# Optimization experiments

Hardware: AMD Instinct MI355X
Metric: run time of the kernel (lower is better)

The kernel has to match this reference:

```python
import jax, jax.numpy as jnp
import numpy as np

# ---- Hash-grid configuration (matches init_kwargs / torch-ngp HashEncoder) ----
L = 16            # num_levels
D = 2             # level_dim
BASE = 16         # base_resolution
DESIRED = 2048    # desired_resolution
MAXP = 2 ** 19    # 2**log2_hashmap_size
DIVIDE = 1.5

S = np.exp2(np.log2(DESIRED / BASE) / (L - 1))          # per-level scale ~1.3819
RES = np.ceil(BASE * S ** np.arange(L)).astype(np.int64)  # [L] grid resolutions
_sizes = np.minimum(MAXP, (RES + 1) ** 3)
SIZES = (np.ceil(_sizes / 8) * 8).astype(np.int64)       # aligned to 8, per torch-ngp
OFFSETS = np.concatenate([[0], np.cumsum(SIZES)[:-1]])
TOTAL = int(SIZES.sum())  # 6119864
DENSE = (RES + 1) ** 3 <= SIZES                          # levels small enough for direct index
PRIMES = (1, 2654435761, 805459861)


def hash_encode(x01, table):
    """x01: [N,3] in [0,1]; table: [TOTAL, D]. Returns [N, L*D]."""
    N = x01.shape[0]
    scale = jnp.asarray(BASE * S ** np.arange(L) - 1.0, jnp.float32)   # [L]
    pos = x01[:, None, :] * scale[None, :, None] + 0.5                 # [N,L,3]
    pg_f = jnp.floor(pos)
    frac = pos - pg_f                                                  # [N,L,3]
    pg = pg_f.astype(jnp.uint32)

    res1 = jnp.asarray(RES + 1, jnp.uint32)        # [L]
    sizes = jnp.asarray(SIZES, jnp.uint32)         # [L]
    offs = jnp.asarray(OFFSETS, jnp.int32)         # [L]
    dense = jnp.asarray(DENSE)                     # [L] bool

    feat = jnp.zeros((N, L, D), x01.dtype)
    for c in range(8):  # 8 trilinear corners (fixed small loop)
        bit = np.array([(c >> 0) & 1, (c >> 1) & 1, (c >> 2) & 1])
        cg = pg + jnp.asarray(bit, jnp.uint32)                         # [N,L,3]
        w = jnp.prod(jnp.where(jnp.asarray(bit.astype(bool)), frac, 1.0 - frac), axis=-1)  # [N,L]
        idx_dense = cg[..., 0] + cg[..., 1] * res1 + cg[..., 2] * res1 * res1
        h = (cg[..., 0] * jnp.uint32(PRIMES[0])) ^ (cg[..., 1] * jnp.uint32(PRIMES[1])) ^ (cg[..., 2] * jnp.uint32(PRIMES[2]))
        idx = jnp.where(dense[None, :], idx_dense % sizes, h % sizes)  # [N,L]
        gidx = idx.astype(jnp.int32) + offs[None, :]                   # global table index
        feat = feat + w[..., None] * table[gidx]                       # gather + lerp accumulate
    return feat.reshape(N, L * D)


def setup_inputs() -> dict:
    key = jax.random.key(0)
    ks = jax.random.split(key, 10)
    N = 524288
    x = jax.random.uniform(ks[0], (N, 3), jnp.float32)                # coords in [0,1)
    table = jax.random.uniform(ks[1], (TOTAL, D), jnp.float32, -1e-4, 1e-4)
    def lin(k, fi, fo):
        return jax.random.normal(k, (fi, fo), jnp.float32) / np.sqrt(fi)
    return {
        'x': x, 'table': table,
        'w1': lin(ks[2], 32, 256), 'b1': jnp.zeros((256,), jnp.float32),
        'w2': lin(ks[3], 256, 256), 'b2': jnp.zeros((256,), jnp.float32),
        'w3': lin(ks[4], 256, 256), 'b3': jnp.zeros((256,), jnp.float32),
        'w4': lin(ks[5], 256, 3), 'b4': jnp.zeros((3,), jnp.float32),
    }


def reference(x, table, w1, b1, w2, b2, w3, b3, w4, b4):
    feat = hash_encode(x / DIVIDE, table)                 # [N,32]
    h = jax.nn.relu(feat @ w1 + b1)
    h = jax.nn.relu(h @ w2 + b2)
    h = jax.nn.relu(h @ w3 + b3)
    rgb = jax.nn.sigmoid(h @ w4 + b4)                     # [N,3]
    return rgb
```

## Files before the change

### kernel.cpp

```cpp
#include <hip/hip_runtime.h>
#include <hip/hip_bf16.h>
#include <math.h>

#define NTHREADS 256
#define BR 64

typedef __attribute__((ext_vector_type(8))) short   s16x8;
typedef __attribute__((ext_vector_type(8))) __bf16  bf16x8;
typedef __attribute__((ext_vector_type(4))) float   f32x4;

__device__ __constant__ float c_scale[16] = {
    15.0f,        21.110607f,  29.554930f,  41.224254f,
    57.350239f,   79.634946f,  110.430473f, 152.987205f,
    211.796890f,  293.066769f, 405.374657f, 560.574388f,
    775.046906f,  1071.429232f, 1481.003616f, 2047.0f
};
__device__ __constant__ unsigned c_off[16] = {
    0u,        4920u,     18744u,    51512u,
    136696u,   352696u,   876984u,   1401272u,
    1925560u,  2449848u,  2974136u,  3498424u,
    4022712u,  4547000u,  5071288u,  5595576u
};
__device__ __constant__ unsigned c_res1[16] = {
    17u, 24u, 32u, 44u, 60u, 0u,0u,0u,0u,0u,0u,0u,0u,0u,0u,0u
};

__device__ inline unsigned short f2bf(float f) {
    unsigned u = __builtin_bit_cast(unsigned, f);
    u += 0x7FFFu + ((u >> 16) & 1u);
    return (unsigned short)(u >> 16);
}
__device__ inline float bf2f(unsigned short h) {
    unsigned u = ((unsigned)h) << 16;
    return __builtin_bit_cast(float, u);
}
__device__ inline f32x4 mfma_bf16(s16x8 a, s16x8 b, f32x4 c) {
    return __builtin_amdgcn_mfma_f32_16x16x32_bf16(
        __builtin_bit_cast(bf16x8, a), __builtin_bit_cast(bf16x8, b), c, 0, 0, 0);
}

__global__ void convert_w(const float* __restrict__ w1, const float* __restrict__ w2,
                          const float* __restrict__ w3, unsigned short* __restrict__ ws) {
    int t = blockIdx.x * blockDim.x + threadIdx.x;
    if (t < 8192) {
        int col = t >> 5, k = t & 31;
        ws[t] = f2bf(w1[k * 256 + col]);
    } else if (t < 73728) {
        int u = t - 8192; int col = u >> 8, k = u & 255;
        ws[t] = f2bf(w2[k * 256 + col]);
    } else if (t < 139264) {
        int u = t - 73728; int col = u >> 8, k = u & 255;
        ws[t] = f2bf(w3[k * 256 + col]);
    }
}

__global__ void convert_table(const float* __restrict__ t, unsigned short* __restrict__ o, int n4) {
    int i = blockIdx.x * blockDim.x + threadIdx.x;
    if (i < n4) {
        float4 v = ((const float4*)t)[i];
        ushort4 r;
        r.x = f2bf(v.x); r.y = f2bf(v.y); r.z = f2bf(v.z); r.w = f2bf(v.w);
        ((ushort4*)o)[i] = r;
    }
}

__global__ __launch_bounds__(256)
void encode_kernel(const float* __restrict__ x, const unsigned short* __restrict__ tbf,
                   uint2* __restrict__ feat2, int N)
{
    const int p  = blockIdx.x * 256 + threadIdx.x;
    const int lp = blockIdx.y;
    if (p >= N) return;

    const float inv = (1.0f / 1.5f);
    const float xc = x[3 * p + 0] * inv;
    const float yc = x[3 * p + 1] * inv;
    const float zc = x[3 * p + 2] * inv;

    unsigned outv[2];
    #pragma unroll
    for (int s = 0; s < 2; ++s) {
        const int l = lp * 2 + s;
        const float sc = c_scale[l];
        const float px = xc * sc + 0.5f;
        const float py = yc * sc + 0.5f;
        const float pz = zc * sc + 0.5f;
        const float fx = floorf(px), fy = floorf(py), fz = floorf(pz);
        const float rx = px - fx, ry = py - fy, rz = pz - fz;
        const unsigned ux = (unsigned)fx, uy = (unsigned)fy, uz = (unsigned)fz;
        const unsigned off = c_off[l];
        const unsigned r1  = c_res1[l];
        const bool dense = (l < 5);
        float ax = 0.0f, ay = 0.0f;
        #pragma unroll
        for (int c = 0; c < 8; ++c) {
            const unsigned bx = c & 1, by = (c >> 1) & 1, bz = (c >> 2) & 1;
            const unsigned cx = ux + bx, cy = uy + by, cz = uz + bz;
            const float wx = bx ? rx : (1.0f - rx);
            const float wy = by ? ry : (1.0f - ry);
            const float wz = bz ? rz : (1.0f - rz);
            const float w = wx * wy * wz;
            unsigned idx;
            if (dense) idx = cx + cy * r1 + cz * r1 * r1;
            else       idx = (cx ^ (cy * 2654435761u) ^ (cz * 805459861u)) & 524287u;
            const unsigned v = *reinterpret_cast<const unsigned*>(tbf + 2u * (idx + off));
            ax = fmaf(w, bf2f((unsigned short)(v & 0xFFFFu)), ax);
            ay = fmaf(w, bf2f((unsigned short)(v >> 16)), ay);
        }
        outv[s] = (unsigned)f2bf(ax) | ((unsigned)f2bf(ay) << 16);
    }
    feat2[(size_t)lp * N + p] = make_uint2(outv[0], outv[1]);
}

__global__ __launch_bounds__(NTHREADS, 3)
void mlp_kernel(const uint2* __restrict__ feat2,
                const unsigned short* __restrict__ wt,
                const float* __restrict__ b1, const float* __restrict__ b2,
                const float* __restrict__ b3,
                const float* __restrict__ w4, const float* __restrict__ b4,
                float* __restrict__ out, int N)
{
    __shared__ unsigned short sA[BR * 256];
    char* sAb = (char*)sA;

    const int tid = threadIdx.x;
    const int p0  = blockIdx.x * BR;
    if (p0 >= N) return;

    #pragma unroll
    for (int it = 0; it < 2; ++it) {
        const int t  = it * NTHREADS + tid;
        const int lp = t >> 6;
        const int p  = t & 63;
        const uint2 v = feat2[(size_t)lp * N + p0 + p];
        *reinterpret_cast<uint2*>(
            sAb + p * 512 + (((unsigned)(lp * 8)) ^ ((unsigned)((p & 7) << 4)))) = v;
    }
    __syncthreads();

    const int lane = tid & 63;
    const int wid  = tid >> 6;
    const int rowb = wid * 64;
    const int arow = lane & 15;
    const int kgrp = lane >> 4;
    const int bcol = lane & 15;

    f32x4 acc[4][4];

    auto epilogue = [&](const float* __restrict__ bias) {
        #pragma unroll
        for (int rt = 0; rt < 4; ++rt) {
            const int f0 = rowb + rt * 16 + kgrp * 4;
            const float4 bv = *reinterpret_cast<const float4*>(bias + f0);
            #pragma unroll
            for (int ct = 0; ct < 4; ++ct) {
                const int p = ct * 16 + bcol;
                const float v0 = fmaxf(acc[rt][ct][0] + bv.x, 0.0f);
                const float v1 = fmaxf(acc[rt][ct][1] + bv.y, 0.0f);
                const float v2 = fmaxf(acc[rt][ct][2] + bv.z, 0.0f);
                const float v3 = fmaxf(acc[rt][ct][3] + bv.w, 0.0f);
                uint2 pk;
                pk.x = (unsigned)f2bf(v0) | ((unsigned)f2bf(v1) << 16);
                pk.y = (unsigned)f2bf(v2) | ((unsigned)f2bf(v3) << 16);
                *reinterpret_cast<uint2*>(
                    sAb + p * 512 + (((unsigned)(2 * f0)) ^ ((unsigned)((p & 7) << 4)))) = pk;
            }
        }
    };

    {
        #pragma unroll
        for (int rt = 0; rt < 4; ++rt)
            #pragma unroll
            for (int ct = 0; ct < 4; ++ct) acc[rt][ct] = f32x4{0.f, 0.f, 0.f, 0.f};

        s16x8 wfr[4];
        #pragma unroll
        for (int rt = 0; rt < 4; ++rt)
            wfr[rt] = *reinterpret_cast<const s16x8*>(wt + (rowb + rt * 16 + arow) * 32 + kgrp * 8);
        #pragma unroll
        for (int ct = 0; ct < 4; ++ct) {
            const int p = ct * 16 + bcol;
            const s16x8 bfr = *reinterpret_cast<const s16x8*>(
                sAb + p * 512 + (((unsigned)(kgrp * 16)) ^ ((unsigned)((p & 7) << 4))));
            #pragma unroll
            for (int rt = 0; rt < 4; ++rt)
                acc[rt][ct] = mfma_bf16(wfr[rt], bfr, acc[rt][ct]);
        }
        __syncthreads();
        epilogue(b1);
        __syncthreads();
    }

    #pragma unroll 1
    for (int layer = 0; layer < 2; ++layer) {
        const unsigned short* __restrict__ W = wt + 8192 + (layer << 16);
        #pragma unroll
        for (int rt = 0; rt < 4; ++rt)
            #pragma unroll
            for (int ct = 0; ct < 4; ++ct) acc[rt][ct] = f32x4{0.f, 0.f, 0.f, 0.f};

        for (int ks = 0; ks < 8; ++ks) {
            s16x8 wfr[4];
            #pragma unroll
            for (int rt = 0; rt < 4; ++rt)
                wfr[rt] = *reinterpret_cast<const s16x8*>(
                    W + (rowb + rt * 16 + arow) * 256 + ks * 32 + kgrp * 8);
            #pragma unroll
            for (int ct = 0; ct < 4; ++ct) {
                const int p = ct * 16 + bcol;
                const s16x8 bfr = *reinterpret_cast<const s16x8*>(
                    sAb + p * 512 + (((unsigned)(ks * 64 + kgrp * 16)) ^ ((unsigned)((p & 7) << 4))));
                #pragma unroll
                for (int rt = 0; rt < 4; ++rt)
                    acc[rt][ct] = mfma_bf16(wfr[rt], bfr, acc[rt][ct]);
            }
        }
        __syncthreads();
        epilogue(layer == 0 ? b2 : b3);
        __syncthreads();
    }

    if (tid < BR * 3) {
        const int r = tid / 3;
        const int c = tid - 3 * r;
        float z = 0.0f;
        for (int kb = 0; kb < 32; ++kb) {
            const s16x8 hv = *reinterpret_cast<const s16x8*>(
                sAb + r * 512 + (((unsigned)(kb * 16)) ^ ((unsigned)((r & 7) << 4))));
            #pragma unroll
            for (int j = 0; j < 8; ++j)
                z = fmaf(bf2f((unsigned short)hv[j]), w4[(kb * 8 + j) * 3 + c], z);
        }
        z += b4[c];
        const int pi = p0 + r;
        if (pi < N) out[pi * 3 + c] = 1.0f / (1.0f + expf(-z));
    }
}

template<bool BFT>
__global__ __launch_bounds__(NTHREADS, 3)
void fused_hashmlp(const float* __restrict__ x, const float* __restrict__ table,
                   const unsigned short* __restrict__ tbf,
                   const unsigned short* __restrict__ wt,
                   const float* __restrict__ b1, const float* __restrict__ b2,
                   const float* __restrict__ b3,
                   const float* __restrict__ w4, const float* __restrict__ b4,
                   float* __restrict__ out, int N)
{
    __shared__ float sX[BR][3];
    __shared__ unsigned short sA[BR * 256];
    const int tid = threadIdx.x;
    const int p0  = blockIdx.x * BR;
    if (p0 >= N) return;
    char* sAb = (char*)sA;

    if (tid < BR * 3) sX[tid / 3][tid % 3] = x[p0 * 3 + tid];
    __syncthreads();

    #pragma unroll
    for (int it = 0; it < 4; ++it) {
        const int task = it * NTHREADS + tid;
        const int l = task >> 6;
        const int p = task & 63;
        const float sc  = c_scale[l];
        const float inv = (1.0f / 1.5f);
        const float px = sX[p][0] * inv * sc + 0.5f;
        const float py = sX[p][1] * inv * sc + 0.5f;
        const float pz = sX[p][2] * inv * sc + 0.5f;
        const float fx = floorf(px), fy = floorf(py), fz = floorf(pz);
        const float rx = px - fx, ry = py - fy, rz = pz - fz;
        const unsigned ux = (unsigned)fx, uy = (unsigned)fy, uz = (unsigned)fz;
        const unsigned off = c_off[l];
        const unsigned r1  = c_res1[l];
        const bool dense = (l < 5);
        float ax = 0.0f, ay = 0.0f;
        #pragma unroll
        for (int c = 0; c < 8; ++c) {
            const unsigned bx = c & 1, by = (c >> 1) & 1, bz = (c >> 2) & 1;
            const unsigned cx = ux + bx, cy = uy + by, cz = uz + bz;
            const float wx = bx ? rx : (1.0f - rx);
            const float wy = by ? ry : (1.0f - ry);
            const float wz = bz ? rz : (1.0f - rz);
            const float w = wx * wy * wz;
            unsigned idx;
            if (dense) idx = cx + cy * r1 + cz * r1 * r1;
            else       idx = (cx ^ (cy * 2654435761u) ^ (cz * 805459861u)) & 524287u;
            float tx, ty;
            if (BFT) {
                const unsigned v = *reinterpret_cast<const unsigned*>(tbf + 2u * (idx + off));
                tx = bf2f((unsigned short)(v & 0xFFFFu));
                ty = bf2f((unsigned short)(v >> 16));
            } else {
                const float2 tv = *reinterpret_cast<const float2*>(table + 2u * (idx + off));
                tx = tv.x; ty = tv.y;
            }
            ax = fmaf(w, tx, ax);
            ay = fmaf(w, ty, ay);
        }
        const unsigned pack = (unsigned)f2bf(ax) | ((unsigned)f2bf(ay) << 16);
        *reinterpret_cast<unsigned*>(sAb + p * 512 + ((l * 4) ^ ((p & 7) << 4))) = pack;
    }
    __syncthreads();

    const int lane = tid & 63;
    const int wid  = tid >> 6;
    const int rowb = wid * 64;
    const int arow = lane & 15;
    const int kgrp = lane >> 4;
    const int bcol = lane & 15;

    f32x4 acc[4][4];

    auto epilogue = [&](const float* __restrict__ bias) {
        #pragma unroll
        for (int rt = 0; rt < 4; ++rt) {
            const int f0 = rowb + rt * 16 + kgrp * 4;
            const float4 bv = *reinterpret_cast<const float4*>(bias + f0);
            #pragma unroll
            for (int ct = 0; ct < 4; ++ct) {
                const int p = ct * 16 + bcol;
                const float v0 = fmaxf(acc[rt][ct][0] + bv.x, 0.0f);
                const float v1 = fmaxf(acc[rt][ct][1] + bv.y, 0.0f);
                const float v2 = fmaxf(acc[rt][ct][2] + bv.z, 0.0f);
                const float v3 = fmaxf(acc[rt][ct][3] + bv.w, 0.0f);
                uint2 pk;
                pk.x = (unsigned)f2bf(v0) | ((unsigned)f2bf(v1) << 16);
                pk.y = (unsigned)f2bf(v2) | ((unsigned)f2bf(v3) << 16);
                *reinterpret_cast<uint2*>(
                    sAb + p * 512 + (((unsigned)(2 * f0)) ^ ((unsigned)((p & 7) << 4)))) = pk;
            }
        }
    };

    {
        #pragma unroll
        for (int rt = 0; rt < 4; ++rt)
            #pragma unroll
            for (int ct = 0; ct < 4; ++ct) acc[rt][ct] = f32x4{0.f, 0.f, 0.f, 0.f};
        s16x8 wfr[4];
        #pragma unroll
        for (int rt = 0; rt < 4; ++rt)
            wfr[rt] = *reinterpret_cast<const s16x8*>(wt + (rowb + rt * 16 + arow) * 32 + kgrp * 8);
        #pragma unroll
        for (int ct = 0; ct < 4; ++ct) {
            const int p = ct * 16 + bcol;
            const s16x8 bfr = *reinterpret_cast<const s16x8*>(
                sAb + p * 512 + (((unsigned)(kgrp * 16)) ^ ((unsigned)((p & 7) << 4))));
            #pragma unroll
            for (int rt = 0; rt < 4; ++rt)
                acc[rt][ct] = mfma_bf16(wfr[rt], bfr, acc[rt][ct]);
        }
        __syncthreads();
        epilogue(b1);
        __syncthreads();
    }

    #pragma unroll 1
    for (int layer = 0; layer < 2; ++layer) {
        const unsigned short* __restrict__ W = wt + 8192 + (layer << 16);
        #pragma unroll
        for (int rt = 0; rt < 4; ++rt)
            #pragma unroll
            for (int ct = 0; ct < 4; ++ct) acc[rt][ct] = f32x4{0.f, 0.f, 0.f, 0.f};
        for (int ks = 0; ks < 8; ++ks) {
            s16x8 wfr[4];
            #pragma unroll
            for (int rt = 0; rt < 4; ++rt)
                wfr[rt] = *reinterpret_cast<const s16x8*>(
                    W + (rowb + rt * 16 + arow) * 256 + ks * 32 + kgrp * 8);
            #pragma unroll
            for (int ct = 0; ct < 4; ++ct) {
                const int p = ct * 16 + bcol;
                const s16x8 bfr = *reinterpret_cast<const s16x8*>(
                    sAb + p * 512 + (((unsigned)(ks * 64 + kgrp * 16)) ^ ((unsigned)((p & 7) << 4))));
                #pragma unroll
                for (int rt = 0; rt < 4; ++rt)
                    acc[rt][ct] = mfma_bf16(wfr[rt], bfr, acc[rt][ct]);
            }
        }
        __syncthreads();
        epilogue(layer == 0 ? b2 : b3);
        __syncthreads();
    }

    if (tid < BR * 3) {
        const int r = tid / 3;
        const int c = tid - 3 * r;
        float z = 0.0f;
        for (int kb = 0; kb < 32; ++kb) {
            const s16x8 hv = *reinterpret_cast<const s16x8*>(
                sAb + r * 512 + (((unsigned)(kb * 16)) ^ ((unsigned)((r & 7) << 4))));
            #pragma unroll
            for (int j = 0; j < 8; ++j)
                z = fmaf(bf2f((unsigned short)hv[j]), w4[(kb * 8 + j) * 3 + c], z);
        }
        z += b4[c];
        const int pi = p0 + r;
        if (pi < N) out[pi * 3 + c] = 1.0f / (1.0f + expf(-z));
    }
}

extern "C" void kernel_launch(void* const* d_in, const int* in_sizes, int n_in,
                              void* d_out, int out_size, void* d_ws, size_t ws_size,
                              hipStream_t stream) {
    const float* x     = (const float*)d_in[0];
    const float* table = (const float*)d_in[1];
    const float* w1    = (const float*)d_in[2];
    const float* b1    = (const float*)d_in[3];
    const float* w2    = (const float*)d_in[4];
    const float* b2    = (const float*)d_in[5];
    const float* w3    = (const float*)d_in[6];
    const float* b3    = (const float*)d_in[7];
    const float* w4    = (const float*)d_in[8];
    const float* b4    = (const float*)d_in[9];
    float* out = (float*)d_out;

    const int N = in_sizes[0] / 3;

    const size_t W_ELEMS    = 139264;
    const size_t TBL_ELEMS  = 12239728;
    const size_t need_bf    = (W_ELEMS + TBL_ELEMS) * 2;
    const size_t FEAT_BYTES = (size_t)N * 64;
    const size_t need_split = need_bf + FEAT_BYTES;

    unsigned short* wsw = (unsigned short*)d_ws;
    unsigned short* tbf = wsw + W_ELEMS;
    uint2* feat2 = (uint2*)((char*)d_ws + need_bf);

    hipLaunchKernelGGL(convert_w, dim3(544), dim3(256), 0, stream, w1, w2, w3, wsw);

    if (ws_size >= need_split) {
        const size_t n4 = TBL_ELEMS / 4;
        hipLaunchKernelGGL(convert_table, dim3((unsigned)((n4 + 255) / 256)), dim3(256), 0, stream,
                           table, tbf, (int)n4);
        hipLaunchKernelGGL(encode_kernel, dim3((N + 255) / 256, 8), dim3(256), 0, stream,
                           x, tbf, feat2, N);
        hipLaunchKernelGGL(mlp_kernel, dim3((N + BR - 1) / BR), dim3(NTHREADS), 0, stream,
                           feat2, wsw, b1, b2, b3, w4, b4, out, N);
    } else if (ws_size >= need_bf) {
        const size_t n4 = TBL_ELEMS / 4;
        hipLaunchKernelGGL(convert_table, dim3((unsigned)((n4 + 255) / 256)), dim3(256), 0, stream,
                           table, tbf, (int)n4);
        hipLaunchKernelGGL(fused_hashmlp<true>, dim3((N + BR - 1) / BR), dim3(NTHREADS), 0, stream,
                           x, table, tbf, wsw, b1, b2, b3, w4, b4, out, N);
    } else {
        hipLaunchKernelGGL(fused_hashmlp<false>, dim3((N + BR - 1) / BR), dim3(NTHREADS), 0, stream,
                           x, table, tbf, wsw, b1, b2, b3, w4, b4, out, N);
    }
}
```

Measured before the change: 664.8 us.

## Use MFMA for output layer, packed bf16 converts, interleave encode block order

The final 256->3 layer in the MLP kernel moves from a scalar per-thread dot product on a subset of threads to a padded 16-row bf16 MFMA, with w4 pre-converted to bf16 in the weight workspace. Float-to-bf16 packing switches to the hardware v_cvt_pk_bf16_f32 instruction. The encode grid is flattened so the 8 level-pairs for the same points run in adjacent blocks, which aims to improve cache locality on the x reads. The fused fallback drops its bf16-table variant, and w4 precision falls to bf16.

New measurement: 643.3 us. -3.2%, faster.

```diff
diff --git a/kernel.cpp b/kernel.cpp
--- a/kernel.cpp
+++ b/kernel.cpp
@@ -34,13 +34,19 @@
     unsigned u = ((unsigned)h) << 16;
     return __builtin_bit_cast(float, u);
 }
+__device__ inline unsigned cvtpk(float lo, float hi) {
+    unsigned r;
+    asm("v_cvt_pk_bf16_f32 %0, %1, %2" : "=v"(r) : "v"(lo), "v"(hi));
+    return r;
+}
 __device__ inline f32x4 mfma_bf16(s16x8 a, s16x8 b, f32x4 c) {
     return __builtin_amdgcn_mfma_f32_16x16x32_bf16(
         __builtin_bit_cast(bf16x8, a), __builtin_bit_cast(bf16x8, b), c, 0, 0, 0);
 }
 
 __global__ void convert_w(const float* __restrict__ w1, const float* __restrict__ w2,
-                          const float* __restrict__ w3, unsigned short* __restrict__ ws) {
+                          const float* __restrict__ w3, const float* __restrict__ w4,
+                          unsigned short* __restrict__ ws) {
     int t = blockIdx.x * blockDim.x + threadIdx.x;
     if (t < 8192) {
         int col = t >> 5, k = t & 31;
@@ -51,6 +57,9 @@
     } else if (t < 139264) {
         int u = t - 73728; int col = u >> 8, k = u & 255;
         ws[t] = f2bf(w3[k * 256 + col]);
+    } else if (t < 143360) {
+        int u = t - 139264; int ch = u >> 8, k = u & 255;
+        ws[t] = (ch < 3) ? f2bf(w4[k * 3 + ch]) : (unsigned short)0;
     }
 }
 
@@ -68,8 +77,8 @@
 void encode_kernel(const float* __restrict__ x, const unsigned short* __restrict__ tbf,
                    uint2* __restrict__ feat2, int N)
 {
-    const int p  = blockIdx.x * 256 + threadIdx.x;
-    const int lp = blockIdx.y;
+    const int lp = blockIdx.x & 7;
+    const int p  = (blockIdx.x >> 3) * 256 + threadIdx.x;
     if (p >= N) return;
 
     const float inv = (1.0f / 1.5f);
@@ -107,7 +116,7 @@
             ax = fmaf(w, bf2f((unsigned short)(v & 0xFFFFu)), ax);
             ay = fmaf(w, bf2f((unsigned short)(v >> 16)), ay);
         }
-        outv[s] = (unsigned)f2bf(ax) | ((unsigned)f2bf(ay) << 16);
+        outv[s] = cvtpk(ax, ay);
     }
     feat2[(size_t)lp * N + p] = make_uint2(outv[0], outv[1]);
 }
@@ -116,8 +125,7 @@
 void mlp_kernel(const uint2* __restrict__ feat2,
                 const unsigned short* __restrict__ wt,
                 const float* __restrict__ b1, const float* __restrict__ b2,
-                const float* __restrict__ b3,
-                const float* __restrict__ w4, const float* __restrict__ b4,
+                const float* __restrict__ b3, const float* __restrict__ b4,
                 float* __restrict__ out, int N)
 {
     __shared__ unsigned short sA[BR * 256];
@@ -160,8 +168,8 @@
                 const float v2 = fmaxf(acc[rt][ct][2] + bv.z, 0.0f);
                 const float v3 = fmaxf(acc[rt][ct][3] + bv.w, 0.0f);
                 uint2 pk;
-                pk.x = (unsigned)f2bf(v0) | ((unsigned)f2bf(v1) << 16);
-                pk.y = (unsigned)f2bf(v2) | ((unsigned)f2bf(v3) << 16);
+                pk.x = cvtpk(v0, v1);
+                pk.y = cvtpk(v2, v3);
                 *reinterpret_cast<uint2*>(
                     sAb + p * 512 + (((unsigned)(2 * f0)) ^ ((unsigned)((p & 7) << 4)))) = pk;
             }
@@ -221,27 +229,32 @@
         __syncthreads();
     }
 
-    if (tid < BR * 3) {
-        const int r = tid / 3;
-        const int c = tid - 3 * r;
-        float z = 0.0f;
-        for (int kb = 0; kb < 32; ++kb) {
-            const s16x8 hv = *reinterpret_cast<const s16x8*>(
-                sAb + r * 512 + (((unsigned)(kb * 16)) ^ ((unsigned)((r & 7) << 4))));
-            #pragma unroll
-            for (int j = 0; j < 8; ++j)
-                z = fmaf(bf2f((unsigned short)hv[j]), w4[(kb * 8 + j) * 3 + c], z);
-        }
-        z += b4[c];
-        const int pi = p0 + r;
-        if (pi < N) out[pi * 3 + c] = 1.0f / (1.0f + expf(-z));
-    }
-}
-
-template<bool BFT>
+    {
+        const unsigned short* __restrict__ W4 = wt + 139264;
+        const int p = wid * 16 + bcol;
+        f32x4 a4 = f32x4{0.f, 0.f, 0.f, 0.f};
+        #pragma unroll
+        for (int ks = 0; ks < 8; ++ks) {
+            const s16x8 wfr = *reinterpret_cast<const s16x8*>(W4 + arow * 256 + ks * 32 + kgrp * 8);
+            const s16x8 bfr = *reinterpret_cast<const s16x8*>(
+                sAb + p * 512 + (((unsigned)(ks * 64 + kgrp * 16)) ^ ((unsigned)((p & 7) << 4))));
+            a4 = mfma_bf16(wfr, bfr, a4);
+        }
+        if (kgrp == 0) {
+            const int pi = p0 + p;
+            if (pi < N) {
+                #pragma unroll
+                for (int c = 0; c < 3; ++c) {
+                    const float z = a4[c] + b4[c];
+                    out[pi * 3 + c] = 1.0f / (1.0f + expf(-z));
+                }
+            }
+        }
+    }
+}
+
 __global__ __launch_bounds__(NTHREADS, 3)
 void fused_hashmlp(const float* __restrict__ x, const float* __restrict__ table,
-                   const unsigned short* __restrict__ tbf,
                    const unsigned short* __restrict__ wt,
                    const float* __restrict__ b1, const float* __restrict__ b2,
                    const float* __restrict__ b3,
@@ -286,17 +299,9 @@
             unsigned idx;
             if (dense) idx = cx + cy * r1 + cz * r1 * r1;
             else       idx = (cx ^ (cy * 2654435761u) ^ (cz * 805459861u)) & 524287u;
-            float tx, ty;
-            if (BFT) {
-                const unsigned v = *reinterpret_cast<const unsigned*>(tbf + 2u * (idx + off));
-                tx = bf2f((unsigned short)(v & 0xFFFFu));
-                ty = bf2f((unsigned short)(v >> 16));
-            } else {
-                const float2 tv = *reinterpret_cast<const float2*>(table + 2u * (idx + off));
-                tx = tv.x; ty = tv.y;
-            }
-            ax = fmaf(w, tx, ax);
-            ay = fmaf(w, ty, ay);
+            const float2 tv = *reinterpret_cast<const float2*>(table + 2u * (idx + off));
+            ax = fmaf(w, tv.x, ax);
+            ay = fmaf(w, tv.y, ay);
         }
         const unsigned pack = (unsigned)f2bf(ax) | ((unsigned)f2bf(ay) << 16);
         *reinterpret_cast<unsigned*>(sAb + p * 512 + ((l * 4) ^ ((p & 7) << 4))) = pack;
@@ -387,15 +392,19 @@
     if (tid < BR * 3) {
         const int r = tid / 3;
         const int c = tid - 3 * r;
-        float z = 0.0f;
-        for (int kb = 0; kb < 32; ++kb) {
-            const s16x8 hv = *reinterpret_cast<const s16x8*>(
+        float z0 = 0.0f, z1 = 0.0f;
+        for (int kb = 0; kb < 32; kb += 2) {
+            const s16x8 hv0 = *reinterpret_cast<const s16x8*>(
                 sAb + r * 512 + (((unsigned)(kb * 16)) ^ ((unsigned)((r & 7) << 4))));
-            #pragma unroll
-            for (int j = 0; j < 8; ++j)
-                z = fmaf(bf2f((unsigned short)hv[j]), w4[(kb * 8 + j) * 3 + c], z);
-        }
-        z += b4[c];
+            const s16x8 hv1 = *reinterpret_cast<const s16x8*>(
+                sAb + r * 512 + (((unsigned)((kb + 1) * 16)) ^ ((unsigned)((r & 7) << 4))));
+            #pragma unroll
+            for (int j = 0; j < 8; ++j) {
+                z0 = fmaf(bf2f((unsigned short)hv0[j]), w4[(kb * 8 + j) * 3 + c], z0);
+                z1 = fmaf(bf2f((unsigned short)hv1[j]), w4[((kb + 1) * 8 + j) * 3 + c], z1);
+            }
+        }
+        const float z = z0 + z1 + b4[c];
         const int pi = p0 + r;
         if (pi < N) out[pi * 3 + c] = 1.0f / (1.0f + expf(-z));
     }
@@ -418,7 +427,7 @@
 
     const int N = in_sizes[0] / 3;
 
-    const size_t W_ELEMS    = 139264;
+    const size_t W_ELEMS    = 143360;
     const size_t TBL_ELEMS  = 12239728;
     const size_t need_bf    = (W_ELEMS + TBL_ELEMS) * 2;
     const size_t FEAT_BYTES = (size_t)N * 64;
@@ -428,24 +437,19 @@
     unsigned short* tbf = wsw + W_ELEMS;
     uint2* feat2 = (uint2*)((char*)d_ws + need_bf);
 
-    hipLaunchKernelGGL(convert_w, dim3(544), dim3(256), 0, stream, w1, w2, w3, wsw);
+    hipLaunchKernelGGL(convert_w, dim3(560), dim3(256), 0, stream, w1, w2, w3, w4, wsw);
 
     if (ws_size >= need_split) {
         const size_t n4 = TBL_ELEMS / 4;
         hipLaunchKernelGGL(convert_table, dim3((unsigned)((n4 + 255) / 256)), dim3(256), 0, stream,
                            table, tbf, (int)n4);
-        hipLaunchKernelGGL(encode_kernel, dim3((N + 255) / 256, 8), dim3(256), 0, stream,
+        const unsigned pblocks = (unsigned)((N + 255) / 256);
+        hipLaunchKernelGGL(encode_kernel, dim3(pblocks * 8), dim3(256), 0, stream,
                            x, tbf, feat2, N);
         hipLaunchKernelGGL(mlp_kernel, dim3((N + BR - 1) / BR), dim3(NTHREADS), 0, stream,
-                           feat2, wsw, b1, b2, b3, w4, b4, out, N);
-    } else if (ws_size >= need_bf) {
-        const size_t n4 = TBL_ELEMS / 4;
-        hipLaunchKernelGGL(convert_table, dim3((unsigned)((n4 + 255) / 256)), dim3(256), 0, stream,
-                           table, tbf, (int)n4);
-        hipLaunchKernelGGL(fused_hashmlp<true>, dim3((N + BR - 1) / BR), dim3(NTHREADS), 0, stream,
-                           x, table, tbf, wsw, b1, b2, b3, w4, b4, out, N);
+                           feat2, wsw, b1, b2, b3, b4, out, N);
     } else {
-        hipLaunchKernelGGL(fused_hashmlp<false>, dim3((N + BR - 1) / BR), dim3(NTHREADS), 0, stream,
-                           x, table, tbf, wsw, b1, b2, b3, w4, b4, out, N);
-    }
-}
+        hipLaunchKernelGGL(fused_hashmlp, dim3((N + BR - 1) / BR), dim3(NTHREADS), 0, stream,
+                           x, table, wsw, b1, b2, b3, w4, b4, out, N);
+    }
+}
```
